# Optimization experiments

Measured on AMD Instinct MI355X. Metric: run time of the kernel, lower is better.

Reference implementation:

```python
import jax, jax.numpy as jnp
import numpy as np

B, T, D, NH, DK = 2, 2048, 1024, 16, 64
EPS = 1e-6

def proj_H(z):
    return z - z.mean(axis=-1, keepdims=True)

def to_clr(p):
    return proj_H(jnp.log(p + EPS))

def setup_inputs() -> dict:
    key = jax.random.key(0)
    ks = jax.random.split(key, 9)
    p = jax.random.uniform(ks[0], (B, T, D), dtype=jnp.float32)
    # xavier_uniform with gain=0.8 for square-ish [in,out] matrices
    def xavier(k, fan_in, fan_out):
        bound = 0.8 * np.sqrt(6.0 / (fan_in + fan_out))
        return jax.random.uniform(k, (fan_in, fan_out), minval=-bound, maxval=bound, dtype=jnp.float32)
    H = NH * DK
    Wq = xavier(ks[1], D, H); bq = jnp.zeros((H,), jnp.float32)
    Wk = xavier(ks[2], D, H); bk = jnp.zeros((H,), jnp.float32)
    Wv = xavier(ks[3], D, H); bv = jnp.zeros((H,), jnp.float32)
    Wo = xavier(ks[4], H, D); bo = jnp.zeros((D,), jnp.float32)
    return {"p": p, "Wq": Wq, "bq": bq, "Wk": Wk, "bk": bk,
            "Wv": Wv, "bv": bv, "Wo": Wo, "bo": bo}

def reference(p, Wq, bq, Wk, bk, Wv, bv, Wo, bo):
    z = to_clr(p)                                   # [B,T,D]
    # projections with H-projection epilogue, reshaped to [B,T,NH,DK]
    q = proj_H(z @ Wq + bq).reshape(B, T, NH, DK)
    k = proj_H(z @ Wk + bk).reshape(B, T, NH, DK)
    v = proj_H(z @ Wv + bv).reshape(B, T, NH, DK)
    att = jnp.einsum('bihd,bjhd->bhij', q, k) / jnp.sqrt(jnp.float32(DK))
    w = jax.nn.softmax(att, axis=-1)                # dropout is identity in eval
    z_out = jnp.einsum('bhij,bjhd->bihd', w, v).reshape(B, T, NH * DK)
    z_out = proj_H(z_out @ Wo + bo)
    return jax.nn.softmax(z_out, axis=-1)           # from_clr
```

## Files before the change

kernel.cpp:

```cpp
#include <hip/hip_runtime.h>

typedef unsigned short u16;
typedef __attribute__((ext_vector_type(8))) short short8_t;
typedef __attribute__((ext_vector_type(8))) _Float16 half8_t;
typedef __attribute__((ext_vector_type(4))) float f32x4;
typedef __attribute__((ext_vector_type(16))) float f32x16;
typedef __attribute__((ext_vector_type(4))) int int4v;

#define BB    2
#define TT    2048
#define DD    1024
#define NHEAD 16
#define DKH   64
#define HH    1024
#define MR    4096
#define CLR_EPS 1e-6f
#define QSCALE_CONST 0.18033688011112042f

#define O_WQKVT  0ull
#define O_WOT    6291456ull
#define O_WMEAN  8388608ull
#define O_BQKV   8404992ull
#define O_BO     8417280ull
#define O_Z      8421376ull
#define O_QKV    16809984ull
#define O_VT     41975808ull
#define O_ZOUT   50364416ull
#define O_LOGITS O_QKV

__device__ __forceinline__ u16 f2h(float f) {
  _Float16 h = (_Float16)f;
  return __builtin_bit_cast(u16, h);
}
__device__ __forceinline__ float h2f(u16 x) {
  return (float)__builtin_bit_cast(_Float16, x);
}

__device__ __forceinline__ f32x4 mfma16(short8_t a, short8_t b, f32x4 c) {
  return __builtin_amdgcn_mfma_f32_16x16x32_f16(
      __builtin_bit_cast(half8_t, a), __builtin_bit_cast(half8_t, b), c, 0, 0, 0);
}
__device__ __forceinline__ f32x16 mfma32(short8_t a, short8_t b, f32x16 c) {
  return __builtin_amdgcn_mfma_f32_32x32x16_f16(
      __builtin_bit_cast(half8_t, a), __builtin_bit_cast(half8_t, b), c, 0, 0, 0);
}

typedef const __attribute__((address_space(1))) unsigned int as1_u32_t;
typedef __attribute__((address_space(3))) unsigned int as3_u32_t;

__device__ __forceinline__ void async16(const void* g, void* l) {
  __builtin_amdgcn_global_load_lds((as1_u32_t*)g, (as3_u32_t*)l, 16, 0, 0);
}

__device__ __forceinline__ void stage2(const u16* __restrict__ G, int base_row,
                                       int r0, int r1, int k0, int schk, u16* lds) {
  const int c0 = k0 + ((schk ^ (r0 & 7)) << 3);
  const int c1 = k0 + ((schk ^ (r1 & 7)) << 3);
  async16(G + (size_t)(base_row + r0) * 1024 + c0, lds + r0 * 64 + schk * 8);
  async16(G + (size_t)(base_row + r1) * 1024 + c1, lds + r1 * 64 + schk * 8);
}

__device__ __forceinline__ short8_t ldfrag(const u16* buf, int row, int kh, int lane) {
  const int byte = (row * 128 + ((kh * 32 + ((lane >> 4) << 3)) << 1)) ^ ((row & 7) << 4);
  return *(const short8_t*)((const char*)buf + byte);
}

__global__ __launch_bounds__(256) void wprep_mean(
    const float* __restrict__ Wq, const float* __restrict__ Wk,
    const float* __restrict__ Wv, const float* __restrict__ Wo,
    const float* __restrict__ bq, const float* __restrict__ bk,
    const float* __restrict__ bv, const float* __restrict__ bo,
    float* __restrict__ wmean, float* __restrict__ bqkv_p, float* __restrict__ bo_p) {
  __shared__ float sb[4];
  const int bid = blockIdx.x, tid = threadIdx.x;
  if (bid < 4096) {
    const int m = bid >> 10, d = bid & 1023;
    const float* Wm = (m == 0) ? Wq : (m == 1) ? Wk : (m == 2) ? Wv : Wo;
    float4 x = ((const float4*)(Wm + (size_t)d * 1024))[tid];
    float s = x.x + x.y + x.z + x.w;
    #pragma unroll
    for (int dd = 32; dd; dd >>= 1) s += __shfl_xor(s, dd);
    if ((tid & 63) == 0) sb[tid >> 6] = s;
    __syncthreads();
    if (tid == 0) wmean[bid] = (sb[0] + sb[1] + sb[2] + sb[3]) * (1.f / 1024.f);
  } else {
    const int j = bid - 4096;
    const float* bb = (j == 0) ? bq : (j == 1) ? bk : (j == 2) ? bv : bo;
    float4 x = ((const float4*)bb)[tid];
    float s = x.x + x.y + x.z + x.w;
    #pragma unroll
    for (int dd = 32; dd; dd >>= 1) s += __shfl_xor(s, dd);
    if ((tid & 63) == 0) sb[tid >> 6] = s;
    __syncthreads();
    const float mean = (sb[0] + sb[1] + sb[2] + sb[3]) * (1.f / 1024.f);
    float* dst = (j < 3) ? (bqkv_p + j * 1024) : bo_p;
    float4 o = {x.x - mean, x.y - mean, x.z - mean, x.w - mean};
    ((float4*)dst)[tid] = o;
  }
}

__global__ __launch_bounds__(256) void wprep_trans(
    const float* __restrict__ Wq, const float* __restrict__ Wk,
    const float* __restrict__ Wv, const float* __restrict__ Wo,
    const float* __restrict__ wmean, u16* __restrict__ wqkvt, u16* __restrict__ wot) {
  __shared__ float tl[64][65];
  const int tj = blockIdx.x, ti = blockIdx.y, m = blockIdx.z;
  const int tid = threadIdx.x;
  const float* Wm = (m == 0) ? Wq : (m == 1) ? Wk : (m == 2) ? Wv : Wo;
  const int d0 = ti * 64, h0 = tj * 64;
  #pragma unroll
  for (int rr = 0; rr < 4; ++rr) {
    const int r = (tid >> 4) + rr * 16;
    float4 x = *(const float4*)(Wm + (size_t)(d0 + r) * 1024 + h0 + ((tid & 15) << 2));
    const float mu = wmean[m * 1024 + d0 + r];
    tl[r][(tid & 15) * 4 + 0] = x.x - mu;
    tl[r][(tid & 15) * 4 + 1] = x.y - mu;
    tl[r][(tid & 15) * 4 + 2] = x.z - mu;
    tl[r][(tid & 15) * 4 + 3] = x.w - mu;
  }
  __syncthreads();
  #pragma unroll
  for (int rr = 0; rr < 2; ++rr) {
    const int hh = (tid >> 3) + rr * 32;
    const int cd = (tid & 7) << 3;
    short8_t v;
    #pragma unroll
    for (int i = 0; i < 8; ++i) v[i] = (short)f2h(tl[cd + i][hh]);
    u16* dst = (m < 3) ? (wqkvt + ((size_t)(m * 1024 + h0 + hh)) * 1024 + d0 + cd)
                       : (wot + ((size_t)(h0 + hh)) * 1024 + d0 + cd);
    *(short8_t*)dst = v;
  }
}

__global__ __launch_bounds__(256) void clr_kernel(const float* __restrict__ p, u16* __restrict__ z) {
  __shared__ float sb[4];
  const int r = blockIdx.x, tid = threadIdx.x;
  float4 x = ((const float4*)(p + (size_t)r * 1024))[tid];
  float l0 = __logf(x.x + CLR_EPS), l1 = __logf(x.y + CLR_EPS);
  float l2 = __logf(x.z + CLR_EPS), l3 = __logf(x.w + CLR_EPS);
  float s = l0 + l1 + l2 + l3;
  #pragma unroll
  for (int dd = 32; dd; dd >>= 1) s += __shfl_xor(s, dd);
  if ((tid & 63) == 0) sb[tid >> 6] = s;
  __syncthreads();
  const float mu = (sb[0] + sb[1] + sb[2] + sb[3]) * (1.f / 1024.f);
  ushort4 o;
  o.x = f2h(l0 - mu); o.y = f2h(l1 - mu); o.z = f2h(l2 - mu); o.w = f2h(l3 - mu);
  ((ushort4*)(z + (size_t)r * 1024))[tid] = o;
}

__global__ __launch_bounds__(512, 2) void gemm_qkv_8ph(
    const u16* __restrict__ A, const u16* __restrict__ Bt, const float* __restrict__ bias,
    u16* __restrict__ qkv, u16* __restrict__ vt) {
  __shared__ u16 As[2][256 * 64];
  __shared__ u16 Bs[2][256 * 64];
  const int tid = threadIdx.x, lane = tid & 63, wid = tid >> 6;
  const int wm = wid >> 2, wn = wid & 3;
  const int id = blockIdx.x;
  const int nid = (id & 7) * 24 + (id >> 3);
  const int m0 = (nid / 12) * 256, n0 = (nid % 12) * 256;
  const int srow = tid >> 3, schk = tid & 7;
  const int l15 = lane & 15, lg4 = (lane >> 4) << 2;

  f32x4 acc[8][4] = {};

  stage2(Bt, n0, srow, srow + 64, 0, schk, &Bs[0][0]);
  stage2(Bt, n0, srow + 128, srow + 192, 0, schk, &Bs[0][0]);
  stage2(A, m0, srow, srow + 128, 0, schk, &As[0][0]);
  stage2(A, m0, srow + 64, srow + 192, 0, schk, &As[0][0]);
  asm volatile("s_waitcnt vmcnt(0)" ::: "memory");
  __builtin_amdgcn_s_barrier();

  short8_t afr[4], bfr[4];
  for (int t = 0; t < 16; ++t) {
    const int cur = t & 1;
    const int k0n = ((t + 1) & 15) * 64;
    const u16* Ab = &As[cur][0];
    const u16* Bb_ = &Bs[cur][0];
    u16* Asn = &As[cur ^ 1][0];
    u16* Bsn = &Bs[cur ^ 1][0];

    #pragma unroll
    for (int j = 0; j < 4; ++j) bfr[j] = ldfrag(Bb_, wn * 64 + j * 16 + l15, 0, lane);
    #pragma unroll
    for (int i = 0; i < 4; ++i) afr[i] = ldfrag(Ab, wm * 128 + i * 16 + l15, 0, lane);
    stage2(Bt, n0, srow, srow + 64, k0n, schk, Bsn);
    stage2(Bt, n0, srow + 128, srow + 192, k0n, schk, Bsn);
    __builtin_amdgcn_s_barrier();
    asm volatile("s_waitcnt lgkmcnt(0)" ::: "memory");
    __builtin_amdgcn_sched_barrier(0);
    __builtin_amdgcn_s_setprio(1);
    #pragma unroll
    for (int i = 0; i < 4; ++i)
      #pragma unroll
      for (int j = 0; j < 4; ++j)
        acc[i][j] = mfma16(afr[i], bfr[j], acc[i][j]);
    __builtin_amdgcn_s_setprio(0);
    __builtin_amdgcn_s_barrier();

    #pragma unroll
    for (int i = 0; i < 4; ++i) afr[i] = ldfrag(Ab, wm * 128 + 64 + i * 16 + l15, 0, lane);
    stage2(A, m0, srow, srow + 128, k0n, schk, Asn);
    stage2(A, m0, srow + 64, srow + 192, k0n, schk, Asn);
    __builtin_amdgcn_s_barrier();
    asm volatile("s_waitcnt lgkmcnt(0)" ::: "memory");
    __builtin_amdgcn_sched_barrier(0);
    __builtin_amdgcn_s_setprio(1);
    #pragma unroll
    for (int i = 0; i < 4; ++i)
      #pragma unroll
      for (int j = 0; j < 4; ++j)
        acc[4 + i][j] = mfma16(afr[i], bfr[j], acc[4 + i][j]);
    __builtin_amdgcn_s_setprio(0);
    __builtin_amdgcn_s_barrier();

    #pragma unroll
    for (int j = 0; j < 4; ++j) bfr[j] = ldfrag(Bb_, wn * 64 + j * 16 + l15, 1, lane);
    #pragma unroll
    for (int i = 0; i < 4; ++i) afr[i] = ldfrag(Ab, wm * 128 + i * 16 + l15, 1, lane);
    __builtin_amdgcn_s_barrier();
    asm volatile("s_waitcnt lgkmcnt(0)" ::: "memory");
    __builtin_amdgcn_sched_barrier(0);
    __builtin_amdgcn_s_setprio(1);
    #pragma unroll
    for (int i = 0; i < 4; ++i)
      #pragma unroll
      for (int j = 0; j < 4; ++j)
        acc[i][j] = mfma16(afr[i], bfr[j], acc[i][j]);
    __builtin_amdgcn_s_setprio(0);
    __builtin_amdgcn_s_barrier();

    #pragma unroll
    for (int i = 0; i < 4; ++i) afr[i] = ldfrag(Ab, wm * 128 + 64 + i * 16 + l15, 1, lane);
    asm volatile("s_waitcnt vmcnt(0)" ::: "memory");
    __builtin_amdgcn_s_barrier();
    asm volatile("s_waitcnt lgkmcnt(0)" ::: "memory");
    __builtin_amdgcn_sched_barrier(0);
    __builtin_amdgcn_s_setprio(1);
    #pragma unroll
    for (int i = 0; i < 4; ++i)
      #pragma unroll
      for (int j = 0; j < 4; ++j)
        acc[4 + i][j] = mfma16(afr[i], bfr[j], acc[4 + i][j]);
    __builtin_amdgcn_s_setprio(0);
    __builtin_amdgcn_s_barrier();
  }

  if (n0 < 2048) {
    const float sc = (n0 < 1024) ? QSCALE_CONST : 1.0f;
    #pragma unroll
    for (int j = 0; j < 4; ++j) {
      const int col = n0 + wn * 64 + j * 16 + l15;
      const float bb = bias[col];
      #pragma unroll
      for (int i = 0; i < 8; ++i) {
        const int rowb = m0 + wm * 128 + i * 16 + lg4;
        #pragma unroll
        for (int r = 0; r < 4; ++r)
          qkv[(size_t)(rowb + r) * 3072 + col] = f2h((acc[i][j][r] + bb) * sc);
      }
    }
  } else {
    const int h = (n0 - 2048 + wn * 64) >> 6;
    #pragma unroll
    for (int j = 0; j < 4; ++j) {
      const int dk = j * 16 + l15;
      const float bb = bias[n0 + wn * 64 + dk];
      #pragma unroll
      for (int i = 0; i < 8; ++i) {
        const int rowb = m0 + wm * 128 + i * 16 + lg4;
        const int b = rowb >> 11, tq = rowb & 2047;
        const int k5 = tq & 31;
        const int pos = (tq & ~31) + (k5 & 16) + ((k5 & 4) << 1) + ((k5 & 8) >> 1);
        ushort4 pk;
        pk.x = f2h(acc[i][j][0] + bb);
        pk.y = f2h(acc[i][j][1] + bb);
        pk.z = f2h(acc[i][j][2] + bb);
        pk.w = f2h(acc[i][j][3] + bb);
        *(ushort4*)(vt + ((size_t)((b * NHEAD + h) * 64 + dk)) * TT + pos) = pk;
      }
    }
  }
}

__global__ __launch_bounds__(256) void gemm_bt(
    const u16* __restrict__ A, const u16* __restrict__ Bt, const float* __restrict__ bias,
    float* __restrict__ Cout, int Ndim, int Kdim) {
  __shared__ u16 As[128 * 64];
  __shared__ u16 Bs[128 * 64];
  const int tid = threadIdx.x;
  const int lane = tid & 63, wid = tid >> 6;
  const int m0 = blockIdx.y * 128, n0 = blockIdx.x * 128;
  const int wm = wid >> 1, wn = wid & 1;
  const int srow = tid >> 3, schk = tid & 7;
  f32x4 acc[4][4] = {};

  for (int k0 = 0; k0 < Kdim; k0 += 64) {
    __syncthreads();
    #pragma unroll
    for (int rr = 0; rr < 4; ++rr) {
      const int row = srow + rr * 32;
      const int gcol = k0 + ((schk ^ (row & 7)) << 3);
      async16(A + (size_t)(m0 + row) * Kdim + gcol, &As[row * 64 + schk * 8]);
      async16(Bt + (size_t)(n0 + row) * Kdim + gcol, &Bs[row * 64 + schk * 8]);
    }
    __syncthreads();
    #pragma unroll
    for (int kk = 0; kk < 2; ++kk) {
      short8_t af[4], bf[4];
      #pragma unroll
      for (int i = 0; i < 4; ++i) {
        af[i] = ldfrag(As, wm * 64 + i * 16 + (lane & 15), kk, lane);
        bf[i] = ldfrag(Bs, wn * 64 + i * 16 + (lane & 15), kk, lane);
      }
      #pragma unroll
      for (int i = 0; i < 4; ++i)
        #pragma unroll
        for (int j = 0; j < 4; ++j)
          acc[i][j] = mfma16(af[i], bf[j], acc[i][j]);
    }
  }
  #pragma unroll
  for (int j = 0; j < 4; ++j) {
    const int col = n0 + wn * 64 + j * 16 + (lane & 15);
    const float bb = bias[col];
    #pragma unroll
    for (int i = 0; i < 4; ++i) {
      const int rowb = m0 + wm * 64 + i * 16 + ((lane >> 4) << 2);
      #pragma unroll
      for (int r = 0; r < 4; ++r)
        Cout[(size_t)(rowb + r) * Ndim + col] = acc[i][j][r] + bb;
    }
  }
}

__global__ __launch_bounds__(512, 2) void attn_kernel(
    const u16* __restrict__ qkv, const u16* __restrict__ vt, u16* __restrict__ zout) {
  __shared__ char smem[65536];
  const int qb = blockIdx.x, h = blockIdx.y, b = blockIdx.z;
  const int tid = threadIdx.x, lane = tid & 63, w = tid >> 6;
  const int qw = w & 3, ks = w >> 2;
  const int hl = lane >> 5, l31 = lane & 31;
  const int swz = (l31 & 7) << 4;
  const int q0 = qb * 256 + qw * 64;

  short8_t qf[2][4];
  #pragma unroll
  for (int qt = 0; qt < 2; ++qt)
    #pragma unroll
    for (int c = 0; c < 4; ++c)
      qf[qt][c] = *(const short8_t*)(qkv + (size_t)(b * TT + q0 + qt * 32 + l31) * 3072
                                     + h * 64 + c * 16 + hl * 8);

  const int sr0 = qw * 16 + (lane >> 3);
  const int schk = lane & 7;
  const int scol = (schk ^ (sr0 & 7)) << 3;
  const int dof = sr0 * 128 + schk * 16;
  char* kls = smem + ks * 16384;
  char* vls = smem + 32768 + ks * 16384;
  const u16* kg = qkv + 1024 + (size_t)h * 64;
  const u16* vg = vt + ((size_t)(b * NHEAD + h) * 64 + sr0) * (size_t)TT;

  {
    const int kbase = ks * 1024;
    async16(kg + (size_t)(b * TT + kbase + sr0) * 3072 + scol, kls + dof);
    async16(kg + (size_t)(b * TT + kbase + sr0 + 8) * 3072 + scol, kls + dof + 1024);
    async16(vg + kbase + scol, vls + dof);
    async16(vg + (size_t)8 * TT + kbase + scol, vls + dof + 1024);
  }

  f32x16 o[2][2] = {};
  f32x16 lb[2] = {};
  short8_t ones;
  #pragma unroll
  for (int i = 0; i < 8; ++i) ones[i] = (short)0x3C00;

  for (int it = 0; it < 16; ++it) {
    __syncthreads();
    if (it < 15) {
      const int kbase = ks * 1024 + (it + 1) * 64;
      const int bo = ((it + 1) & 1) * 8192;
      async16(kg + (size_t)(b * TT + kbase + sr0) * 3072 + scol, kls + bo + dof);
      async16(kg + (size_t)(b * TT + kbase + sr0 + 8) * 3072 + scol, kls + bo + dof + 1024);
      async16(vg + kbase + scol, vls + bo + dof);
      async16(vg + (size_t)8 * TT + kbase + scol, vls + bo + dof + 1024);
    }
    const char* Kb = kls + (it & 1) * 8192;
    const char* Vb = vls + (it & 1) * 8192;

    #pragma unroll
    for (int kt = 0; kt < 2; ++kt) {
      f32x16 s[2] = {};
      #pragma unroll
      for (int c = 0; c < 4; ++c) {
        const int krow = kt * 32 + l31;
        const short8_t kfr = *(const short8_t*)(Kb + krow * 128 + ((c * 32 + hl * 16) ^ swz));
        s[0] = mfma32(kfr, qf[0][c], s[0]);
        s[1] = mfma32(kfr, qf[1][c], s[1]);
      }
      #pragma unroll
      for (int qt = 0; qt < 2; ++qt)
        #pragma unroll
        for (int r = 0; r < 16; ++r) {
          float pv;
          asm("v_exp_f32 %0, %1" : "=v"(pv) : "v"(s[qt][r]));
          s[qt][r] = pv;
        }
      #pragma unroll
      for (int cc = 0; cc < 2; ++cc) {
        short8_t pa[2];
        #pragma unroll
        for (int qt = 0; qt < 2; ++qt) {
          int w0 = __builtin_bit_cast(int, __builtin_amdgcn_cvt_pkrtz(s[qt][8 * cc + 0], s[qt][8 * cc + 1]));
          int w1 = __builtin_bit_cast(int, __builtin_amdgcn_cvt_pkrtz(s[qt][8 * cc + 2], s[qt][8 * cc + 3]));
          int w2 = __builtin_bit_cast(int, __builtin_amdgcn_cvt_pkrtz(s[qt][8 * cc + 4], s[qt][8 * cc + 5]));
          int w3 = __builtin_bit_cast(int, __builtin_amdgcn_cvt_pkrtz(s[qt][8 * cc + 6], s[qt][8 * cc + 7]));
          int4v fw = {w0, w1, w2, w3};
          pa[qt] = __builtin_bit_cast(short8_t, fw);
          lb[qt] = mfma32(pa[qt], ones, lb[qt]);
        }
        const int cb = kt * 64 + cc * 32 + hl * 16;
        #pragma unroll
        for (int dkt = 0; dkt < 2; ++dkt) {
          const int vrow = dkt * 32 + l31;
          const short8_t vfr = *(const short8_t*)(Vb + vrow * 128 + (cb ^ swz));
          o[0][dkt] = mfma32(pa[0], vfr, o[0][dkt]);
          o[1][dkt] = mfma32(pa[1], vfr, o[1][dkt]);
        }
      }
    }
  }

  __syncthreads();
  const int slot = qw * 64 + lane;
  if (ks == 1) {
    u16* ro = (u16*)(smem + slot * 136);
    #pragma unroll
    for (int qt = 0; qt < 2; ++qt)
      #pragma unroll
      for (int dkt = 0; dkt < 2; ++dkt)
        #pragma unroll
        for (int r = 0; r < 16; ++r)
          ro[(qt * 2 + dkt) * 16 + r] = f2h(o[qt][dkt][r]);
    u16* rl = (u16*)(smem + 36864 + slot * 72);
    #pragma unroll
    for (int qt = 0; qt < 2; ++qt)
      #pragma unroll
      for (int r = 0; r < 16; ++r)
        rl[qt * 16 + r] = f2h(lb[qt][r]);
  }
  __syncthreads();
  if (ks == 0) {
    const u16* ro = (const u16*)(smem + slot * 136);
    const u16* rl = (const u16*)(smem + 36864 + slot * 72);
    #pragma unroll
    for (int qt = 0; qt < 2; ++qt) {
      #pragma unroll
      for (int r = 0; r < 16; ++r) lb[qt][r] += h2f(rl[qt * 16 + r]);
      #pragma unroll
      for (int dkt = 0; dkt < 2; ++dkt)
        #pragma unroll
        for (int r = 0; r < 16; ++r) o[qt][dkt][r] += h2f(ro[(qt * 2 + dkt) * 16 + r]);
    }
    #pragma unroll
    for (int qt = 0; qt < 2; ++qt) {
      float rlv[16];
      #pragma unroll
      for (int r = 0; r < 16; ++r) rlv[r] = 1.f / lb[qt][r];
      #pragma unroll
      for (int dkt = 0; dkt < 2; ++dkt) {
        const int col = h * 64 + dkt * 32 + l31;
        #pragma unroll
        for (int r = 0; r < 16; ++r) {
          const int rowg = b * TT + q0 + qt * 32 + (r & 3) + 8 * (r >> 2) + 4 * hl;
          zout[(size_t)rowg * 1024 + col] = f2h(o[qt][dkt][r] * rlv[r]);
        }
      }
    }
  }
}

__global__ __launch_bounds__(256) void softmax_rows(const float* __restrict__ logits,
                                                    float* __restrict__ out) {
  __shared__ float sb[8];
  const int r = blockIdx.x, tid = threadIdx.x;
  float4 x = ((const float4*)(logits + (size_t)r * 1024))[tid];
  float mx = fmaxf(fmaxf(x.x, x.y), fmaxf(x.z, x.w));
  #pragma unroll
  for (int dd = 32; dd; dd >>= 1) mx = fmaxf(mx, __shfl_xor(mx, dd));
  if ((tid & 63) == 0) sb[tid >> 6] = mx;
  __syncthreads();
  mx = fmaxf(fmaxf(sb[0], sb[1]), fmaxf(sb[2], sb[3]));
  const float e0 = __expf(x.x - mx), e1 = __expf(x.y - mx);
  const float e2 = __expf(x.z - mx), e3 = __expf(x.w - mx);
  float s = e0 + e1 + e2 + e3;
  #pragma unroll
  for (int dd = 32; dd; dd >>= 1) s += __shfl_xor(s, dd);
  __syncthreads();
  if ((tid & 63) == 0) sb[4 + (tid >> 6)] = s;
  __syncthreads();
  s = sb[4] + sb[5] + sb[6] + sb[7];
  const float inv = 1.f / s;
  float4 o = {e0 * inv, e1 * inv, e2 * inv, e3 * inv};
  ((float4*)(out + (size_t)r * 1024))[tid] = o;
}

extern "C" void kernel_launch(void* const* d_in, const int* in_sizes, int n_in,
                              void* d_out, int out_size, void* d_ws, size_t ws_size,
                              hipStream_t stream) {
  (void)in_sizes; (void)n_in; (void)out_size; (void)ws_size;
  const float* p  = (const float*)d_in[0];
  const float* Wq = (const float*)d_in[1];
  const float* bq = (const float*)d_in[2];
  const float* Wk = (const float*)d_in[3];
  const float* bk = (const float*)d_in[4];
  const float* Wv = (const float*)d_in[5];
  const float* bv = (const float*)d_in[6];
  const float* Wo = (const float*)d_in[7];
  const float* bo = (const float*)d_in[8];
  float* out = (float*)d_out;

  char* ws = (char*)d_ws;
  u16*   wqkvt  = (u16*)(ws + O_WQKVT);
  u16*   wot    = (u16*)(ws + O_WOT);
  float* wmean  = (float*)(ws + O_WMEAN);
  float* bqkv_p = (float*)(ws + O_BQKV);
  float* bo_p   = (float*)(ws + O_BO);
  u16*   z      = (u16*)(ws + O_Z);
  u16*   qkv    = (u16*)(ws + O_QKV);
  u16*   vt     = (u16*)(ws + O_VT);
  u16*   zoutb  = (u16*)(ws + O_ZOUT);
  float* logits = (float*)(ws + O_LOGITS);

  wprep_mean<<<4100, 256, 0, stream>>>(Wq, Wk, Wv, Wo, bq, bk, bv, bo, wmean, bqkv_p, bo_p);
  wprep_trans<<<dim3(16, 16, 4), 256, 0, stream>>>(Wq, Wk, Wv, Wo, wmean, wqkvt, wot);
  clr_kernel<<<MR, 256, 0, stream>>>(p, z);
  gemm_qkv_8ph<<<192, 512, 0, stream>>>(z, wqkvt, bqkv_p, qkv, vt);
  attn_kernel<<<dim3(TT / 256, NHEAD, BB), 512, 0, stream>>>(qkv, vt, zoutb);
  gemm_bt<<<dim3(1024 / 128, MR / 128), 256, 0, stream>>>(zoutb, wot, bo_p, logits, 1024, 1024);
  softmax_rows<<<MR, 256, 0, stream>>>(logits, out);
}
```

Measured before the change: 133.1 us.

## Double-buffer gemm_bt LDS tiles and remap attention block ordering

The output-projection GEMM now keeps two LDS buffers and issues the async global loads for the next K tile before computing the current one, with a single waitcnt plus barrier per iteration, so memory latency overlaps the MFMA work. The attention kernel moves to a 1D grid with a custom mapping from block id to (batch, head, query block), which changes which blocks run together and is meant to improve cache locality and spread work across the dies. Double buffering doubles LDS use in gemm_bt, which may lower occupancy. The final iteration issues a redundant wrapped-around prefetch of tile 0.

Result: no change. 135.4 us (+1.8%).

```diff
diff --git a/kernel.cpp b/kernel.cpp
--- a/kernel.cpp
+++ b/kernel.cpp
@@ -286,8 +286,8 @@
 __global__ __launch_bounds__(256) void gemm_bt(
     const u16* __restrict__ A, const u16* __restrict__ Bt, const float* __restrict__ bias,
     float* __restrict__ Cout, int Ndim, int Kdim) {
-  __shared__ u16 As[128 * 64];
-  __shared__ u16 Bs[128 * 64];
+  __shared__ u16 As[2][128 * 64];
+  __shared__ u16 Bs[2][128 * 64];
   const int tid = threadIdx.x;
   const int lane = tid & 63, wid = tid >> 6;
   const int m0 = blockIdx.y * 128, n0 = blockIdx.x * 128;
@@ -295,23 +295,31 @@
   const int srow = tid >> 3, schk = tid & 7;
   f32x4 acc[4][4] = {};
 
-  for (int k0 = 0; k0 < Kdim; k0 += 64) {
-    __syncthreads();
+  auto STG = [&](int k0, int buf) {
     #pragma unroll
     for (int rr = 0; rr < 4; ++rr) {
       const int row = srow + rr * 32;
       const int gcol = k0 + ((schk ^ (row & 7)) << 3);
-      async16(A + (size_t)(m0 + row) * Kdim + gcol, &As[row * 64 + schk * 8]);
-      async16(Bt + (size_t)(n0 + row) * Kdim + gcol, &Bs[row * 64 + schk * 8]);
-    }
-    __syncthreads();
+      async16(A + (size_t)(m0 + row) * Kdim + gcol, &As[buf][row * 64 + schk * 8]);
+      async16(Bt + (size_t)(n0 + row) * Kdim + gcol, &Bs[buf][row * 64 + schk * 8]);
+    }
+  };
+
+  STG(0, 0);
+  asm volatile("s_waitcnt vmcnt(0)" ::: "memory");
+  __builtin_amdgcn_s_barrier();
+
+  const int nt = Kdim >> 6;
+  for (int t = 0; t < nt; ++t) {
+    const int cur = t & 1;
+    STG((((t + 1) & (nt - 1))) << 6, cur ^ 1);
     #pragma unroll
     for (int kk = 0; kk < 2; ++kk) {
       short8_t af[4], bf[4];
       #pragma unroll
       for (int i = 0; i < 4; ++i) {
-        af[i] = ldfrag(As, wm * 64 + i * 16 + (lane & 15), kk, lane);
-        bf[i] = ldfrag(Bs, wn * 64 + i * 16 + (lane & 15), kk, lane);
+        af[i] = ldfrag(&As[cur][0], wm * 64 + i * 16 + (lane & 15), kk, lane);
+        bf[i] = ldfrag(&Bs[cur][0], wn * 64 + i * 16 + (lane & 15), kk, lane);
       }
       #pragma unroll
       for (int i = 0; i < 4; ++i)
@@ -319,7 +327,10 @@
         for (int j = 0; j < 4; ++j)
           acc[i][j] = mfma16(af[i], bf[j], acc[i][j]);
     }
-  }
+    asm volatile("s_waitcnt vmcnt(0)" ::: "memory");
+    __builtin_amdgcn_s_barrier();
+  }
+
   #pragma unroll
   for (int j = 0; j < 4; ++j) {
     const int col = n0 + wn * 64 + j * 16 + (lane & 15);
@@ -337,7 +348,10 @@
 __global__ __launch_bounds__(512, 2) void attn_kernel(
     const u16* __restrict__ qkv, const u16* __restrict__ vt, u16* __restrict__ zout) {
   __shared__ char smem[65536];
-  const int qb = blockIdx.x, h = blockIdx.y, b = blockIdx.z;
+  const int id = blockIdx.x;
+  const int qb = (id >> 3) & 7;
+  const int bh = (id & 7) * 4 + (id >> 6);
+  const int b = bh >> 4, h = bh & 15;
   const int tid = threadIdx.x, lane = tid & 63, w = tid >> 6;
   const int qw = w & 3, ks = w >> 2;
   const int hl = lane >> 5, l31 = lane & 31;
@@ -536,7 +550,7 @@
   wprep_trans<<<dim3(16, 16, 4), 256, 0, stream>>>(Wq, Wk, Wv, Wo, wmean, wqkvt, wot);
   clr_kernel<<<MR, 256, 0, stream>>>(p, z);
   gemm_qkv_8ph<<<192, 512, 0, stream>>>(z, wqkvt, bqkv_p, qkv, vt);
-  attn_kernel<<<dim3(TT / 256, NHEAD, BB), 512, 0, stream>>>(qkv, vt, zoutb);
+  attn_kernel<<<256, 512, 0, stream>>>(qkv, vt, zoutb);
   gemm_bt<<<dim3(1024 / 128, MR / 128), 256, 0, stream>>>(zoutb, wot, bo_p, logits, 1024, 1024);
   softmax_rows<<<MR, 256, 0, stream>>>(logits, out);
 }
```
